# Kernel optimization log

Measured on AMD Instinct MI355X. Metric: run time of the kernel, lower is better.

Reference implementation:

```python
import jax, jax.numpy as jnp
import numpy as np

N_HEADS, N_LEVELS, N_POINTS = 8, 4, 4


def _bilinear(im, grid, H, W):
    # im: [N, D, H*W] flattened level feature, grid: [N, Q, P, 2] in [-1, 1]
    # F.grid_sample bilinear, padding_mode='zeros', align_corners=False
    N, Q, P, _ = grid.shape
    D = im.shape[1]
    gx = ((grid[..., 0] + 1.0) * W - 1.0) * 0.5
    gy = ((grid[..., 1] + 1.0) * H - 1.0) * 0.5
    x0f = jnp.floor(gx)
    y0f = jnp.floor(gy)
    x0 = x0f.astype(jnp.int32)
    y0 = y0f.astype(jnp.int32)
    wx1 = gx - x0f
    wy1 = gy - y0f
    acc = jnp.zeros((N, D, Q * P), im.dtype)
    corners = ((0, 0, (1 - wx1) * (1 - wy1)), (1, 0, wx1 * (1 - wy1)),
               (0, 1, (1 - wx1) * wy1), (1, 1, wx1 * wy1))
    for dx, dy, wgt in corners:
        xi = x0 + dx
        yi = y0 + dy
        valid = (xi >= 0) & (xi < W) & (yi >= 0) & (yi < H)
        idx = jnp.clip(yi, 0, H - 1) * W + jnp.clip(xi, 0, W - 1)
        v = jnp.take_along_axis(im, idx.reshape(N, 1, Q * P), axis=2)  # [N,D,QP]
        acc = acc + v * jnp.where(valid, wgt, 0.0).reshape(N, 1, Q * P)
    return acc.reshape(N, D, Q, P)


def _forward(query, value, reference_points, shapes_np,
             w_off, b_off, w_attn, b_attn, w_val, b_val, w_out, b_out):
    B, Q, E = query.shape
    H_, L, P = N_HEADS, N_LEVELS, N_POINTS
    D = E // H_
    v = (value @ w_val + b_val).reshape(B, -1, H_, D)  # [B, Nv, H, D]
    off = (query @ w_off + b_off).reshape(B, Q, H_, L, P, 2)
    attn = (query @ w_attn + b_attn).reshape(B, Q, H_, L * P)
    attn = jax.nn.softmax(attn, axis=-1).reshape(B, Q, H_, L, P)
    # offset_scale = [W_l, H_l] per level
    scale = jnp.asarray(np.stack([shapes_np[:, 1], shapes_np[:, 0]], -1), jnp.float32)
    locs = reference_points[:, :, None, :, None, :] + off / scale[None, None, None, :, None, :]
    grid = 2.0 * locs - 1.0  # [B, Q, H, L, P, 2]
    starts = np.concatenate([[0], np.cumsum(shapes_np[:, 0] * shapes_np[:, 1])]).astype(int)
    out = jnp.zeros((B * H_, D, Q), query.dtype)
    for lvl in range(L):
        h, w = int(shapes_np[lvl, 0]), int(shapes_np[lvl, 1])
        feat = v[:, starts[lvl]:starts[lvl + 1]]                      # [B, h*w, H, D]
        feat = feat.transpose(0, 2, 3, 1).reshape(B * H_, D, h * w)   # [BH, D, hw]
        g = jnp.transpose(grid[:, :, :, lvl], (0, 2, 1, 3, 4)).reshape(B * H_, Q, P, 2)
        sampled = _bilinear(feat, g, h, w)                            # [BH, D, Q, P]
        wl = jnp.transpose(attn[:, :, :, lvl], (0, 2, 1, 3)).reshape(B * H_, 1, Q, P)
        out = out + (sampled * wl).sum(-1)                            # [BH, D, Q]
    out = out.reshape(B, H_ * D, Q).transpose(0, 2, 1)                # [B, Q, E]
    return out @ w_out + b_out


def setup_inputs() -> dict:
    key = jax.random.key(0)
    ks = jax.random.split(key, 12)
    B, Q, E = 2, 19947, 256
    L, H_, P = N_LEVELS, N_HEADS, N_POINTS
    shapes = jnp.array([[100, 150], [50, 75], [25, 38], [13, 19]], dtype=jnp.int64)
    s = 0.02
    return {
        'query': jax.random.normal(ks[0], (B, Q, E), jnp.float32),
        'value': jax.random.normal(ks[1], (B, Q, E), jnp.float32),
        'reference_points': jax.random.uniform(ks[2], (B, Q, L, 2), jnp.float32),
        'spatial_shapes': shapes,
        'w_off': jax.random.normal(ks[3], (E, H_ * L * P * 2), jnp.float32) * s,
        'b_off': jax.random.normal(ks[4], (H_ * L * P * 2,), jnp.float32) * s,
        'w_attn': jax.random.normal(ks[5], (E, H_ * L * P), jnp.float32) * s,
        'b_attn': jax.random.normal(ks[6], (H_ * L * P,), jnp.float32) * s,
        'w_val': jax.random.normal(ks[7], (E, E), jnp.float32) * s,
        'b_val': jax.random.normal(ks[8], (E,), jnp.float32) * s,
        'w_out': jax.random.normal(ks[9], (E, E), jnp.float32) * s,
        'b_out': jax.random.normal(ks[10], (E,), jnp.float32) * s,
    }


def reference(query, value, reference_points, spatial_shapes,
              w_off, b_off, w_attn, b_attn, w_val, b_val, w_out, b_out):
    shapes_np = np.asarray(spatial_shapes)
    return _forward(query, value, reference_points, shapes_np,
                    w_off, b_off, w_attn, b_attn, w_val, b_val, w_out, b_out)
```

## Files before the change

### kernel.cpp

```cpp
#include <hip/hip_runtime.h>
#include <math.h>

#define B_    2
#define Q_    19947
#define E_    256
#define H_    8
#define D_    32
#define L_    4
#define P_    4

typedef _Float16 f16_t;
typedef f16_t f16x8 __attribute__((ext_vector_type(8)));
typedef f16_t f16x4 __attribute__((ext_vector_type(4)));
typedef float f32x4 __attribute__((ext_vector_type(4)));

__global__ __launch_bounds__(256)
void transpose_all(const float* __restrict__ w_val, const float* __restrict__ w_off,
                   const float* __restrict__ w_attn, const float* __restrict__ w_out,
                   f16_t* __restrict__ WtV, f16_t* __restrict__ WtQ,
                   f16_t* __restrict__ WtO)
{
    const float* in; f16_t* out; int N;
    switch (blockIdx.z) {
        case 0:  in = w_val;  out = WtV;             N = 256; break;
        case 1:  in = w_off;  out = WtQ;             N = 256; break;
        case 2:  in = w_attn; out = WtQ + 256 * 256; N = 128; break;
        default: in = w_out;  out = WtO;             N = 256; break;
    }
    const int nt = blockIdx.x * 32;
    if (nt >= N) return;
    const int kt = blockIdx.y * 32;

    __shared__ float tile[32][33];
    const int x  = threadIdx.x & 31;
    const int y0 = threadIdx.x >> 5;
    #pragma unroll
    for (int p = 0; p < 4; ++p)
        tile[y0 + p * 8][x] = in[(size_t)(kt + y0 + p * 8) * N + nt + x];
    __syncthreads();
    const int kf = kt >> 5;
    #pragma unroll
    for (int p = 0; p < 4; ++p) {
        const int n    = nt + y0 + p * 8;
        const int nf   = n >> 4, l16 = n & 15;
        const int quad = (x >> 3) & 3, e = x & 7;
        out[(size_t)(nf * 8 + kf) * 512 + (quad * 16 + l16) * 8 + e]
            = (f16_t)tile[x][y0 + p * 8];
    }
}

__global__ __launch_bounds__(256, 4)
void gemm_proj(const float* __restrict__ Aval, const float* __restrict__ Aqry,
               const f16_t* __restrict__ WtV, const f16_t* __restrict__ WtQ,
               const float* __restrict__ b_val, const float* __restrict__ b_off,
               const float* __restrict__ b_attn,
               f16_t* __restrict__ v_proj, float* __restrict__ off_b,
               float* __restrict__ attn_b, int M)
{
    __shared__ __align__(16) f16_t As[32][264];

    const int t  = threadIdx.x;
    const int m0 = blockIdx.x * 32;
    const bool isVal = (blockIdx.y == 0);
    const float* __restrict__ Af = isVal ? Aval : Aqry;
    const f16_t* __restrict__ Wt = isVal ? WtV : WtQ;
    const int JW = isVal ? 4 : 6;

    {
        const int r  = t >> 3;
        const int c0 = (t & 7) * 32;
        const int gm = m0 + r;
        #pragma unroll
        for (int u = 0; u < 2; ++u) {
            f16_t tmp[16];
            if (gm < M) {
                #pragma unroll
                for (int q = 0; q < 4; ++q) {
                    const float4 v4 = *(const float4*)(Af + (size_t)gm * 256 + c0 + u * 16 + q * 4);
                    tmp[q*4+0] = (f16_t)v4.x; tmp[q*4+1] = (f16_t)v4.y;
                    tmp[q*4+2] = (f16_t)v4.z; tmp[q*4+3] = (f16_t)v4.w;
                }
            } else {
                #pragma unroll
                for (int q = 0; q < 16; ++q) tmp[q] = (f16_t)0.f;
            }
            *(f16x8*)&As[r][c0 + u * 16]     = *(const f16x8*)&tmp[0];
            *(f16x8*)&As[r][c0 + u * 16 + 8] = *(const f16x8*)&tmp[8];
        }
    }
    __syncthreads();

    const int lane = t & 63;
    const int w    = t >> 6;
    const int quad = lane >> 4, l16 = lane & 15;

    f16x8 af[2][8];
    #pragma unroll
    for (int mi = 0; mi < 2; ++mi)
        #pragma unroll
        for (int kf = 0; kf < 8; ++kf)
            af[mi][kf] = *(const f16x8*)&As[mi * 16 + l16][kf * 32 + quad * 8];

    for (int j = 0; j < JW; ++j) {
        const int nf = (isVal ? w * 4 : w * 6) + j;
        const f16_t* __restrict__ bp = Wt + (size_t)nf * 4096 + lane * 8;

        f32x4 acc0 = {0.f, 0.f, 0.f, 0.f};
        f32x4 acc1 = {0.f, 0.f, 0.f, 0.f};
        #pragma unroll
        for (int kf = 0; kf < 8; ++kf) {
            const f16x8 bfr = *(const f16x8*)(bp + kf * 512);
            acc0 = __builtin_amdgcn_mfma_f32_16x16x32_f16(af[0][kf], bfr, acc0, 0, 0, 0);
            acc1 = __builtin_amdgcn_mfma_f32_16x16x32_f16(af[1][kf], bfr, acc1, 0, 0, 0);
        }

        const int n  = nf * 16 + l16;
        const float bv = isVal ? b_val[n] : (n < 256 ? b_off[n] : b_attn[n - 256]);
        #pragma unroll
        for (int r = 0; r < 4; ++r) {
            const int gm0 = m0 + quad * 4 + r;
            const int gm1 = gm0 + 16;
            if (isVal) {
                if (gm0 < M) v_proj[(size_t)gm0 * 256 + n] = (f16_t)(acc0[r] + bv);
                if (gm1 < M) v_proj[(size_t)gm1 * 256 + n] = (f16_t)(acc1[r] + bv);
            } else if (n < 256) {
                if (gm0 < M) off_b[(size_t)gm0 * 256 + n] = acc0[r] + bv;
                if (gm1 < M) off_b[(size_t)gm1 * 256 + n] = acc1[r] + bv;
            } else {
                if (gm0 < M) attn_b[(size_t)gm0 * 128 + (n - 256)] = acc0[r] + bv;
                if (gm1 < M) attn_b[(size_t)gm1 * 128 + (n - 256)] = acc1[r] + bv;
            }
        }
    }
}

__global__ __launch_bounds__(256, 4)
void msda_fused(const f16_t* __restrict__ v,
                const float* __restrict__ off,
                const float* __restrict__ attn,
                const float* __restrict__ ref,
                const f16_t* __restrict__ WoT,
                const float* __restrict__ b_out,
                float* __restrict__ out,
                int BQ)
{
    constexpr int SH[4] = {100, 50, 25, 13};
    constexpr int SW[4] = {150, 75, 38, 19};
    constexpr int ST[4] = {0, 15000, 18750, 19700};
    constexpr float LOG2E = 1.4426950408889634f;

    __shared__ __align__(16) f16_t Samp[16][264];

    const int t   = threadIdx.x;
    const int bq0 = blockIdx.x * 16;

    #pragma unroll
    for (int r = 0; r < 2; ++r) {
        const int g    = t >> 2;
        const int qi   = (g >> 3) + r * 8;
        const int h    = g & 7;
        const int lane = t & 3;
        const int bq   = bq0 + qi;

        float acc[8] = {0.f, 0.f, 0.f, 0.f, 0.f, 0.f, 0.f, 0.f};

        if (bq < BQ) {
            const f16x8* __restrict__ vp = (const f16x8*)v;
            const unsigned vb = (bq >= Q_ ? (unsigned)Q_ * 32u : 0u)
                              + (unsigned)(h * 4 + lane);
            const float* __restrict__ offp  = off  + (size_t)bq * 256 + h * 32;
            const float* __restrict__ attnp = attn + (size_t)bq * 128 + h * 16;

            float aw[16];
            #pragma unroll
            for (int i = 0; i < 4; ++i) {
                const float4 x = *(const float4*)(attnp + i * 4);
                aw[i*4+0] = x.x; aw[i*4+1] = x.y; aw[i*4+2] = x.z; aw[i*4+3] = x.w;
            }
            float mx = aw[0];
            #pragma unroll
            for (int i = 1; i < 16; ++i) mx = fmaxf(mx, aw[i]);
            const float mb = mx * LOG2E;
            float sum = 0.f;
            #pragma unroll
            for (int i = 0; i < 16; ++i) {
                aw[i] = exp2f(fmaf(aw[i], LOG2E, -mb));
                sum += aw[i];
            }
            const float inv = 1.f / sum;
            #pragma unroll
            for (int i = 0; i < 16; ++i) aw[i] *= inv;

            const float4 r01 = *(const float4*)(ref + (size_t)bq * 8);
            const float4 r23 = *(const float4*)(ref + (size_t)bq * 8 + 4);
            const float rx[4] = {r01.x, r01.z, r23.x, r23.z};
            const float ry[4] = {r01.y, r01.w, r23.y, r23.w};

            #pragma unroll
            for (int l = 0; l < L_; ++l) {
                const float fW = (float)SW[l], fH = (float)SH[l];
                const int   Ww = SW[l], Hh = SH[l], st = ST[l];
                #pragma unroll
                for (int pp = 0; pp < 2; ++pp) {
                    const float4 o2 = *(const float4*)(offp + l * 8 + pp * 4);
                    #pragma unroll
                    for (int q = 0; q < 2; ++q) {
                        const int   p  = pp * 2 + q;
                        const float ox = q ? o2.z : o2.x;
                        const float oy = q ? o2.w : o2.y;
                        const float wA = aw[l * 4 + p];
                        const float gx = fmaf(rx[l], fW, ox) - 0.5f;
                        const float gy = fmaf(ry[l], fH, oy) - 0.5f;
                        const float x0f = floorf(gx), y0f = floorf(gy);
                        const int   x0  = (int)x0f,   y0  = (int)y0f;
                        const float wx1 = gx - x0f,   wy1 = gy - y0f;
                        const float wx0 = 1.f - wx1,  wy0 = 1.f - wy1;

                        const float mxw0 = ((unsigned)x0     < (unsigned)Ww) ? wx0 : 0.f;
                        const float mxw1 = ((unsigned)(x0+1) < (unsigned)Ww) ? wx1 : 0.f;
                        const float myw0 = ((unsigned)y0     < (unsigned)Hh) ? wy0 : 0.f;
                        const float myw1 = ((unsigned)(y0+1) < (unsigned)Hh) ? wy1 : 0.f;
                        const int xc0 = min(max(x0, 0),     Ww - 1);
                        const int xc1 = min(max(x0 + 1, 0), Ww - 1);
                        const int yc0 = min(max(y0, 0),     Hh - 1);
                        const int yc1 = min(max(y0 + 1, 0), Hh - 1);

                        const float w00 = wA * mxw0 * myw0;
                        const float w10 = wA * mxw1 * myw0;
                        const float w01 = wA * mxw0 * myw1;
                        const float w11 = wA * mxw1 * myw1;

                        const unsigned r0 = (unsigned)(st + yc0 * Ww);
                        const unsigned r1 = (unsigned)(st + yc1 * Ww);
                        const f16x8 s00 = vp[vb + (r0 + (unsigned)xc0) * 32u];
                        const f16x8 s10 = vp[vb + (r0 + (unsigned)xc1) * 32u];
                        const f16x8 s01 = vp[vb + (r1 + (unsigned)xc0) * 32u];
                        const f16x8 s11 = vp[vb + (r1 + (unsigned)xc1) * 32u];

                        #pragma unroll
                        for (int c = 0; c < 8; ++c) {
                            acc[c] = fmaf(w00, (float)s00[c], acc[c]);
                            acc[c] = fmaf(w10, (float)s10[c], acc[c]);
                            acc[c] = fmaf(w01, (float)s01[c], acc[c]);
                            acc[c] = fmaf(w11, (float)s11[c], acc[c]);
                        }
                    }
                }
            }
        }

        f16x8 o;
        #pragma unroll
        for (int c = 0; c < 8; ++c) o[c] = (f16_t)acc[c];
        *(f16x8*)&Samp[qi][h * 32 + lane * 8] = o;
    }

    __syncthreads();

    const int lane = t & 63;
    const int w    = t >> 6;
    const int quad = lane >> 4, l16 = lane & 15;

    f16x8 af[8];
    #pragma unroll
    for (int kf = 0; kf < 8; ++kf)
        af[kf] = *(const f16x8*)&Samp[l16][kf * 32 + quad * 8];

    f32x4 acc4[4];
    #pragma unroll
    for (int j = 0; j < 4; ++j) {
        f32x4 z = {0.f, 0.f, 0.f, 0.f};
        acc4[j] = z;
    }

    __builtin_amdgcn_s_setprio(1);
    #pragma unroll
    for (int j = 0; j < 4; ++j) {
        const int nf = w * 4 + j;
        const f16_t* bp = WoT + (size_t)nf * 4096 + lane * 8;
        #pragma unroll
        for (int kf = 0; kf < 8; ++kf) {
            const f16x8 bfr = *(const f16x8*)(bp + kf * 512);
            acc4[j] = __builtin_amdgcn_mfma_f32_16x16x32_f16(af[kf], bfr, acc4[j], 0, 0, 0);
        }
    }
    __builtin_amdgcn_s_setprio(0);

    #pragma unroll
    for (int j = 0; j < 4; ++j) {
        const int n  = w * 64 + j * 16 + l16;
        const float bv = b_out[n];
        #pragma unroll
        for (int r = 0; r < 4; ++r) {
            const int gm = bq0 + quad * 4 + r;
            if (gm < BQ)
                out[(size_t)gm * 256 + n] = acc4[j][r] + bv;
        }
    }
}

extern "C" void kernel_launch(void* const* d_in, const int* in_sizes, int n_in,
                              void* d_out, int out_size, void* d_ws, size_t ws_size,
                              hipStream_t stream)
{
    const float* query  = (const float*)d_in[0];
    const float* value  = (const float*)d_in[1];
    const float* refpts = (const float*)d_in[2];
    const float* w_off  = (const float*)d_in[4];
    const float* b_off  = (const float*)d_in[5];
    const float* w_attn = (const float*)d_in[6];
    const float* b_attn = (const float*)d_in[7];
    const float* w_val  = (const float*)d_in[8];
    const float* b_val  = (const float*)d_in[9];
    const float* w_out  = (const float*)d_in[10];
    const float* b_out  = (const float*)d_in[11];
    float* out = (float*)d_out;

    const int BQ = B_ * Q_;

    char* ws = (char*)d_ws;
    f16_t* v_proj = (f16_t*)ws;                       ws += (size_t)BQ * 256 * 2;
    float* off_b  = (float*)ws;                       ws += (size_t)BQ * 256 * 4;
    float* attn_b = (float*)ws;                       ws += (size_t)BQ * 128 * 4;
    f16_t* WtV    = (f16_t*)ws;                       ws += (size_t)256 * 256 * 2;
    f16_t* WtQ    = (f16_t*)ws;                       ws += (size_t)384 * 256 * 2;
    f16_t* WtO    = (f16_t*)ws;

    const dim3 blk(256);

    transpose_all<<<dim3(8, 8, 4), blk, 0, stream>>>(w_val, w_off, w_attn, w_out,
                                                     WtV, WtQ, WtO);

    const int mg32 = (BQ + 31) / 32;

    gemm_proj<<<dim3(mg32, 2), blk, 0, stream>>>(
        value, query, WtV, WtQ, b_val, b_off, b_attn,
        v_proj, off_b, attn_b, BQ);

    const int mg16 = (BQ + 15) / 16;
    msda_fused<<<dim3(mg16), blk, 0, stream>>>(
        v_proj, off_b, attn_b, refpts, WtO, b_out, out, BQ);
}
```

Baseline: 280.8 us.

## Fuse query offset/attention projection into the sampling kernel via shared memory

The query projection for sampling offsets and attention logits moves out of the projection GEMM kernel and into msda_fused. Each block now computes its 16 rows of offsets and logits with MFMA and keeps them in shared memory, so the fp32 off/attn buffers are no longer written to and read back from global memory. The cost is a larger shared-memory footprint per block (about 25KB for OffAtn plus AS), which may cut occupancy. The sampling kernel also gains an extra MFMA phase and barrier before gathering.

Result: faster. 253.2 us (-9.8%).

```diff
diff --git a/kernel.cpp b/kernel.cpp
--- a/kernel.cpp
+++ b/kernel.cpp
@@ -50,21 +50,14 @@
 }
 
 __global__ __launch_bounds__(256, 4)
-void gemm_proj(const float* __restrict__ Aval, const float* __restrict__ Aqry,
-               const f16_t* __restrict__ WtV, const f16_t* __restrict__ WtQ,
-               const float* __restrict__ b_val, const float* __restrict__ b_off,
-               const float* __restrict__ b_attn,
-               f16_t* __restrict__ v_proj, float* __restrict__ off_b,
-               float* __restrict__ attn_b, int M)
+void gemm_val(const float* __restrict__ Aval, const f16_t* __restrict__ WtV,
+              const float* __restrict__ b_val,
+              f16_t* __restrict__ v_proj, int M)
 {
     __shared__ __align__(16) f16_t As[32][264];
 
     const int t  = threadIdx.x;
     const int m0 = blockIdx.x * 32;
-    const bool isVal = (blockIdx.y == 0);
-    const float* __restrict__ Af = isVal ? Aval : Aqry;
-    const f16_t* __restrict__ Wt = isVal ? WtV : WtQ;
-    const int JW = isVal ? 4 : 6;
 
     {
         const int r  = t >> 3;
@@ -76,7 +69,7 @@
             if (gm < M) {
                 #pragma unroll
                 for (int q = 0; q < 4; ++q) {
-                    const float4 v4 = *(const float4*)(Af + (size_t)gm * 256 + c0 + u * 16 + q * 4);
+                    const float4 v4 = *(const float4*)(Aval + (size_t)gm * 256 + c0 + u * 16 + q * 4);
                     tmp[q*4+0] = (f16_t)v4.x; tmp[q*4+1] = (f16_t)v4.y;
                     tmp[q*4+2] = (f16_t)v4.z; tmp[q*4+3] = (f16_t)v4.w;
                 }
@@ -101,9 +94,10 @@
         for (int kf = 0; kf < 8; ++kf)
             af[mi][kf] = *(const f16x8*)&As[mi * 16 + l16][kf * 32 + quad * 8];
 
-    for (int j = 0; j < JW; ++j) {
-        const int nf = (isVal ? w * 4 : w * 6) + j;
-        const f16_t* __restrict__ bp = Wt + (size_t)nf * 4096 + lane * 8;
+    #pragma unroll
+    for (int j = 0; j < 4; ++j) {
+        const int nf = w * 4 + j;
+        const f16_t* __restrict__ bp = WtV + (size_t)nf * 4096 + lane * 8;
 
         f32x4 acc0 = {0.f, 0.f, 0.f, 0.f};
         f32x4 acc1 = {0.f, 0.f, 0.f, 0.f};
@@ -115,29 +109,23 @@
         }
 
         const int n  = nf * 16 + l16;
-        const float bv = isVal ? b_val[n] : (n < 256 ? b_off[n] : b_attn[n - 256]);
+        const float bv = b_val[n];
         #pragma unroll
         for (int r = 0; r < 4; ++r) {
             const int gm0 = m0 + quad * 4 + r;
             const int gm1 = gm0 + 16;
-            if (isVal) {
-                if (gm0 < M) v_proj[(size_t)gm0 * 256 + n] = (f16_t)(acc0[r] + bv);
-                if (gm1 < M) v_proj[(size_t)gm1 * 256 + n] = (f16_t)(acc1[r] + bv);
-            } else if (n < 256) {
-                if (gm0 < M) off_b[(size_t)gm0 * 256 + n] = acc0[r] + bv;
-                if (gm1 < M) off_b[(size_t)gm1 * 256 + n] = acc1[r] + bv;
-            } else {
-                if (gm0 < M) attn_b[(size_t)gm0 * 128 + (n - 256)] = acc0[r] + bv;
-                if (gm1 < M) attn_b[(size_t)gm1 * 128 + (n - 256)] = acc1[r] + bv;
-            }
+            if (gm0 < M) v_proj[(size_t)gm0 * 256 + n] = (f16_t)(acc0[r] + bv);
+            if (gm1 < M) v_proj[(size_t)gm1 * 256 + n] = (f16_t)(acc1[r] + bv);
         }
     }
 }
 
 __global__ __launch_bounds__(256, 4)
 void msda_fused(const f16_t* __restrict__ v,
-                const float* __restrict__ off,
-                const float* __restrict__ attn,
+                const float* __restrict__ Aqry,
+                const f16_t* __restrict__ WtQ,
+                const float* __restrict__ b_off,
+                const float* __restrict__ b_attn,
                 const float* __restrict__ ref,
                 const f16_t* __restrict__ WoT,
                 const float* __restrict__ b_out,
@@ -149,10 +137,63 @@
     constexpr int ST[4] = {0, 15000, 18750, 19700};
     constexpr float LOG2E = 1.4426950408889634f;
 
-    __shared__ __align__(16) f16_t Samp[16][264];
+    __shared__ __align__(16) float OffAtn[16][392];
+    __shared__ __align__(16) f16_t AS[16][264];
 
     const int t   = threadIdx.x;
     const int bq0 = blockIdx.x * 16;
+
+    {
+        const int r  = t >> 4;
+        const int c0 = (t & 15) * 16;
+        const int gm = bq0 + r;
+        f16_t tmp[16];
+        if (gm < BQ) {
+            #pragma unroll
+            for (int u = 0; u < 4; ++u) {
+                const float4 v4 = *(const float4*)(Aqry + (size_t)gm * 256 + c0 + u * 4);
+                tmp[u*4+0] = (f16_t)v4.x; tmp[u*4+1] = (f16_t)v4.y;
+                tmp[u*4+2] = (f16_t)v4.z; tmp[u*4+3] = (f16_t)v4.w;
+            }
+        } else {
+            #pragma unroll
+            for (int u = 0; u < 16; ++u) tmp[u] = (f16_t)0.f;
+        }
+        *(f16x8*)&AS[r][c0]     = *(const f16x8*)&tmp[0];
+        *(f16x8*)&AS[r][c0 + 8] = *(const f16x8*)&tmp[8];
+    }
+    __syncthreads();
+
+    {
+        const int lane = t & 63;
+        const int w    = t >> 6;
+        const int quad = lane >> 4, l16 = lane & 15;
+
+        f16x8 af[8];
+        #pragma unroll
+        for (int kf = 0; kf < 8; ++kf)
+            af[kf] = *(const f16x8*)&AS[l16][kf * 32 + quad * 8];
+
+        __builtin_amdgcn_s_setprio(1);
+        #pragma unroll
+        for (int j = 0; j < 6; ++j) {
+            const int nf = w * 6 + j;
+            const f16_t* __restrict__ bp = WtQ + (size_t)nf * 4096 + lane * 8;
+            f32x4 a4 = {0.f, 0.f, 0.f, 0.f};
+            #pragma unroll
+            for (int kf = 0; kf < 8; ++kf) {
+                const f16x8 bfr = *(const f16x8*)(bp + kf * 512);
+                a4 = __builtin_amdgcn_mfma_f32_16x16x32_f16(af[kf], bfr, a4, 0, 0, 0);
+            }
+            const int n  = nf * 16 + l16;
+            const float bv = (n < 256) ? b_off[n] : b_attn[n - 256];
+            #pragma unroll
+            for (int r = 0; r < 4; ++r)
+                OffAtn[quad * 4 + r][n] = a4[r] + bv;
+        }
+        __builtin_amdgcn_s_setprio(0);
+    }
+    __syncthreads();
 
     #pragma unroll
     for (int r = 0; r < 2; ++r) {
@@ -168,13 +209,11 @@
             const f16x8* __restrict__ vp = (const f16x8*)v;
             const unsigned vb = (bq >= Q_ ? (unsigned)Q_ * 32u : 0u)
                               + (unsigned)(h * 4 + lane);
-            const float* __restrict__ offp  = off  + (size_t)bq * 256 + h * 32;
-            const float* __restrict__ attnp = attn + (size_t)bq * 128 + h * 16;
 
             float aw[16];
             #pragma unroll
             for (int i = 0; i < 4; ++i) {
-                const float4 x = *(const float4*)(attnp + i * 4);
+                const float4 x = *(const float4*)&OffAtn[qi][256 + h * 16 + i * 4];
                 aw[i*4+0] = x.x; aw[i*4+1] = x.y; aw[i*4+2] = x.z; aw[i*4+3] = x.w;
             }
             float mx = aw[0];
@@ -202,7 +241,7 @@
                 const int   Ww = SW[l], Hh = SH[l], st = ST[l];
                 #pragma unroll
                 for (int pp = 0; pp < 2; ++pp) {
-                    const float4 o2 = *(const float4*)(offp + l * 8 + pp * 4);
+                    const float4 o2 = *(const float4*)&OffAtn[qi][h * 32 + l * 8 + pp * 4];
                     #pragma unroll
                     for (int q = 0; q < 2; ++q) {
                         const int   p  = pp * 2 + q;
@@ -252,7 +291,7 @@
         f16x8 o;
         #pragma unroll
         for (int c = 0; c < 8; ++c) o[c] = (f16_t)acc[c];
-        *(f16x8*)&Samp[qi][h * 32 + lane * 8] = o;
+        *(f16x8*)&AS[qi][h * 32 + lane * 8] = o;
     }
 
     __syncthreads();
@@ -264,7 +303,7 @@
     f16x8 af[8];
     #pragma unroll
     for (int kf = 0; kf < 8; ++kf)
-        af[kf] = *(const f16x8*)&Samp[l16][kf * 32 + quad * 8];
+        af[kf] = *(const f16x8*)&AS[l16][kf * 32 + quad * 8];
 
     f32x4 acc4[4];
     #pragma unroll
@@ -320,8 +359,6 @@
 
     char* ws = (char*)d_ws;
     f16_t* v_proj = (f16_t*)ws;                       ws += (size_t)BQ * 256 * 2;
-    float* off_b  = (float*)ws;                       ws += (size_t)BQ * 256 * 4;
-    float* attn_b = (float*)ws;                       ws += (size_t)BQ * 128 * 4;
     f16_t* WtV    = (f16_t*)ws;                       ws += (size_t)256 * 256 * 2;
     f16_t* WtQ    = (f16_t*)ws;                       ws += (size_t)384 * 256 * 2;
     f16_t* WtO    = (f16_t*)ws;
@@ -333,11 +370,9 @@
 
     const int mg32 = (BQ + 31) / 32;
 
-    gemm_proj<<<dim3(mg32, 2), blk, 0, stream>>>(
-        value, query, WtV, WtQ, b_val, b_off, b_attn,
-        v_proj, off_b, attn_b, BQ);
+    gemm_val<<<dim3(mg32), blk, 0, stream>>>(value, WtV, b_val, v_proj, BQ);
 
     const int mg16 = (BQ + 15) / 16;
     msda_fused<<<dim3(mg16), blk, 0, stream>>>(
-        v_proj, off_b, attn_b, refpts, WtO, b_out, out, BQ);
+        v_proj, query, WtQ, b_off, b_attn, refpts, WtO, b_out, out, BQ);
 }
```
